# Kernel tuning notes

Measured on AMD Instinct MI355X. Metric: run time of the kernel, lower is better.

The kernel has to match this reference:

```python
import jax, jax.numpy as jnp
import numpy as np
from jax import lax

N = 5000            # number of detections
FEAT = 1024         # last-layer feature dim; 1024 + 9 engineered feats = indim 1033
DIMS = [FEAT + 9, 1000, 600, 300, 150, 1]
IOU_THRESH = 0.5
EPS = 2.220446049250313e-16  # sys.float_info.epsilon


def setup_inputs() -> dict:
    key = jax.random.key(0)
    ks = jax.random.split(key, 8 + 3 * len(DIMS))
    H, W = 800.0, 1333.0
    cx = jax.random.uniform(ks[0], (N,), minval=0.0, maxval=W)
    cy = jax.random.uniform(ks[1], (N,), minval=0.0, maxval=H)
    bw = jax.random.uniform(ks[2], (N,), minval=20.0, maxval=250.0)
    bh = jax.random.uniform(ks[3], (N,), minval=20.0, maxval=250.0)
    x1 = jnp.clip(cx - bw / 2, 0.0, W - 2)
    y1 = jnp.clip(cy - bh / 2, 0.0, H - 2)
    x2 = jnp.clip(cx + bw / 2, x1 + 1, W)
    y2 = jnp.clip(cy + bh / 2, y1 + 1, H)
    inp = {
        'multi_bboxes': jnp.stack([x1, y1, x2, y2], axis=1),
        'cls_score': jax.random.uniform(ks[4], (N, 2)),
        'last_layer_feats': jax.random.normal(ks[5], (N, FEAT)),
        'img_shape': jnp.array([H, W], jnp.float32),
    }
    # PermEqui2_mean params: Gamma (weight+bias) and Lambda (weight only)
    ki = 6
    for i, (din, dout) in enumerate(zip(DIMS[:-1], DIMS[1:])):
        s = 1.0 / np.sqrt(din)
        inp[f'Wg{i+1}'] = jax.random.uniform(ks[ki], (dout, din), minval=-s, maxval=s); ki += 1
        inp[f'bg{i+1}'] = jax.random.uniform(ks[ki], (dout,), minval=-s, maxval=s); ki += 1
        inp[f'Wl{i+1}'] = jax.random.uniform(ks[ki], (dout, din), minval=-s, maxval=s); ki += 1
    return inp


def _greedy_cluster(ious, thresh):
    # Sequential greedy IoU clustering (NMS-like). assign[i] = index of cluster seed.
    n = ious.shape[0]

    def step(carry, inp):
        is_c, assign = carry
        j, row = inp
        seed = is_c[j]
        hit = row > thresh
        member = seed & hit & is_c
        assign = jnp.where(member, j, assign)
        is_c = is_c & ~(seed & hit)
        return (is_c, assign), None

    init = (jnp.ones(n, bool), jnp.zeros(n, jnp.int32))
    (_, assign), _ = lax.scan(step, init, (jnp.arange(n, dtype=jnp.int32), ious))
    return assign


def _forward(multi_bboxes, cls_score, last_layer_feats, img_shape, params):
    n = multi_bboxes.shape[0]
    scores = cls_score[:, 1]
    order = jnp.argsort(-scores)
    scores = scores[order]
    bboxes = multi_bboxes[order]
    feats = last_layer_feats[order]

    x1, y1, x2, y2 = bboxes[:, 0], bboxes[:, 1], bboxes[:, 2], bboxes[:, 3]
    # pairwise IoU with the +1 pixel convention from bbox_overlaps
    iw = jnp.clip(jnp.minimum(x2[:, None], x2[None, :]) - jnp.maximum(x1[:, None], x1[None, :]) + 1, 0)
    ih = jnp.clip(jnp.minimum(y2[:, None], y2[None, :]) - jnp.maximum(y1[:, None], y1[None, :]) + 1, 0)
    area = (x2 - x1 + 1) * (y2 - y1 + 1)
    overlap = iw * ih
    ious = overlap / (area[:, None] + area[None, :] - overlap)

    assign = _greedy_cluster(lax.stop_gradient(ious), IOU_THRESH)
    counts = jax.ops.segment_sum(jnp.ones(n, jnp.float32), assign, num_segments=n)
    cden = jnp.maximum(counts, 1.0)

    Himg, Wimg = img_shape[0], img_shape[1]
    # source double-normalizes: width = (x2/W - x1/W)/W, height = (y2/H - y1/H)/H
    width = (x2 / Wimg - x1 / Wimg) / Wimg
    height = (y2 / Himg - y1 / Himg) / Himg
    areaf = width * height
    ar = width / (height + EPS)
    x = jnp.concatenate([
        bboxes, feats,
        width[:, None], height[:, None], ar[:, None], areaf[:, None], scores[:, None],
    ], axis=1)  # [n, 1033]

    def perm_equi(x, Wg, bg, Wl):
        # xm = per-set mean; x*Gamma^T + b - (xm*Lambda^T), gathered back per box
        xm = jax.ops.segment_sum(x, assign, num_segments=n) / cden[:, None]
        return x @ Wg.T + bg - (xm @ Wl.T)[assign]

    for i in range(5):
        x = jax.nn.elu(perm_equi(x, params[f'Wg{i+1}'], params[f'bg{i+1}'], params[f'Wl{i+1}']))

    # source skips singleton sets (nonzero().squeeze() -> 0-dim): mask them out
    valid = counts[assign] >= 2.0
    return jnp.where(valid[:, None], x, 0.0)  # [n, 1] per-box set logits


def reference(multi_bboxes, cls_score, last_layer_feats, img_shape,
              Wg1, bg1, Wl1, Wg2, bg2, Wl2, Wg3, bg3, Wl3,
              Wg4, bg4, Wl4, Wg5, bg5, Wl5):
    params = {'Wg1': Wg1, 'bg1': bg1, 'Wl1': Wl1, 'Wg2': Wg2, 'bg2': bg2, 'Wl2': Wl2,
              'Wg3': Wg3, 'bg3': bg3, 'Wl3': Wl3, 'Wg4': Wg4, 'bg4': bg4, 'Wl4': Wl4,
              'Wg5': Wg5, 'bg5': bg5, 'Wl5': Wl5}
    return _forward(multi_bboxes, cls_score, last_layer_feats, img_shape, params)
```

## Files before the change

kernel.cpp:

```cpp
#include <hip/hip_runtime.h>
#include <cstdint>
#include <cstddef>

#define N_BOX 5000
#define NW    80
#define LDX   1040
#define LDZ   2048
#define LDYM  1000
#define LDW   1040
#define LDAB  2080
#define NCHUNK ((N_BOX + 63) / 64)
#define RT    ((N_BOX + 255) / 256)

typedef short bf16x8 __attribute__((ext_vector_type(8)));
typedef float f32x4v __attribute__((ext_vector_type(4)));
typedef unsigned short u16x8 __attribute__((ext_vector_type(8)));

__device__ __forceinline__ float fence_f(float x) { asm volatile("" : "+v"(x)); return x; }

__device__ __forceinline__ unsigned short f2bf(float x) {
    unsigned u = __builtin_bit_cast(unsigned, x);
    unsigned r = (u + 0x7FFFu + ((u >> 16) & 1u)) >> 16;
    return (unsigned short)r;
}
__device__ __forceinline__ float bf2f(unsigned short h) {
    unsigned u = ((unsigned)h) << 16;
    return __builtin_bit_cast(float, u);
}

__global__ void rank_partial_kernel(const float* __restrict__ cls, int* __restrict__ rank) {
    __shared__ float sj[256];
    int t = threadIdx.x;
    int jbase = blockIdx.y * 256;
    int jg = jbase + t;
    sj[t] = (jg < N_BOX) ? cls[2 * jg + 1] : 0.0f;
    __syncthreads();
    int i = blockIdx.x * 256 + t;
    if (i >= N_BOX) return;
    float si = cls[2 * i + 1];
    int jmax = (N_BOX - jbase < 256) ? (N_BOX - jbase) : 256;
    int r = 0;
    for (int k = 0; k < jmax; ++k) {
        float sjv = sj[k];
        int j = jbase + k;
        r += (sjv > si) || (sjv == si && j < i);
    }
    atomicAdd(&rank[i], r);
}

__global__ void rank_scatter_kernel(const int* __restrict__ rank, int* __restrict__ ord) {
    int i = blockIdx.x * blockDim.x + threadIdx.x;
    if (i < N_BOX) ord[rank[i]] = i;
}

__global__ void gather_kernel(const float* __restrict__ bb, const float* __restrict__ cls,
                              const float* __restrict__ feats, const float* __restrict__ img,
                              const int* __restrict__ ord,
                              float* __restrict__ X0, float* __restrict__ sb,
                              unsigned short* __restrict__ A2) {
    int r = blockIdx.x;
    if (r >= N_BOX) {
        unsigned short* dst = A2 + (size_t)r * LDAB;
        for (int k = threadIdx.x; k < 2048; k += blockDim.x) dst[k] = 0;
        return;
    }
    int i = ord[r];
    float x1 = bb[4 * i + 0], y1 = bb[4 * i + 1], x2 = bb[4 * i + 2], y2 = bb[4 * i + 3];
    float H = img[0], W = img[1];
    float sc = cls[2 * i + 1];
    if (threadIdx.x == 0) {
        sb[0 * N_BOX + r] = x1;
        sb[1 * N_BOX + r] = y1;
        sb[2 * N_BOX + r] = x2;
        sb[3 * N_BOX + r] = y2;
        sb[4 * N_BOX + r] = (x2 - x1 + 1.0f) * (y2 - y1 + 1.0f);
        sb[5 * N_BOX + r] = sc;
    }
    float width  = (x2 / W - x1 / W) / W;
    float height = (y2 / H - y1 / H) / H;
    float ar     = width / (height + 2.220446049250313e-16f);
    float areaf  = width * height;
    float* row = X0 + (size_t)r * LDX;
    unsigned short* a2row = A2 + (size_t)r * LDAB;
    for (int o = threadIdx.x; o < LDX; o += blockDim.x) {
        float v;
        if (o < 4)          v = (o == 0) ? x1 : (o == 1) ? y1 : (o == 2) ? x2 : y2;
        else if (o < 1028)  v = feats[(size_t)i * 1024 + (o - 4)];
        else if (o == 1028) v = width;
        else if (o == 1029) v = height;
        else if (o == 1030) v = ar;
        else if (o == 1031) v = areaf;
        else if (o == 1032) v = sc;
        else                v = 0.0f;
        row[o] = v;
        if (o >= 4 && o < 1028) {
            int k = o - 4;
            unsigned short hi = f2bf(v);
            a2row[k] = hi;
            a2row[1024 + k] = f2bf(v - bf2f(hi));
        }
    }
}

__global__ void mask_kernel(const float* __restrict__ sb, unsigned long long* __restrict__ mask,
                            unsigned long long* __restrict__ diag, int* __restrict__ counts) {
    int j = blockIdx.x;
    if (threadIdx.x == 0) counts[j] = 0;
    const float* X1 = sb;
    const float* Y1 = sb + N_BOX;
    const float* X2 = sb + 2 * N_BOX;
    const float* Y2 = sb + 3 * N_BOX;
    const float* AR = sb + 4 * N_BOX;
    float xj1 = X1[j], yj1 = Y1[j], xj2 = X2[j], yj2 = Y2[j], aj = AR[j];
    int lane = threadIdx.x & 63;
    int wave = threadIdx.x >> 6;
    int nwav = blockDim.x >> 6;
    int dw = j >> 6;
    for (int w = wave; w < NW; w += nwav) {
        int i = w * 64 + lane;
        bool pred = false;
        if (i < N_BOX) {
            float iw = fmaxf(fminf(xj2, X2[i]) - fmaxf(xj1, X1[i]) + 1.0f, 0.0f);
            float ih = fmaxf(fminf(yj2, Y2[i]) - fmaxf(yj1, Y1[i]) + 1.0f, 0.0f);
            float ov = fence_f(iw * ih);
            float denom = fence_f((aj + AR[i]) - ov);
            pred = (ov / denom) > 0.5f;
        }
        unsigned long long b = __ballot(pred);
        if (lane == 0) {
            mask[(size_t)j * NW + w] = b;
            if (w == dw) diag[j] = b;
        }
    }
}

__device__ __forceinline__ void nms_body(const unsigned long long* __restrict__ mask,
                                         const unsigned long long* __restrict__ diag,
                                         unsigned long long* __restrict__ keep,
                                         unsigned long long* supp,
                                         unsigned long long* keep_sh,
                                         unsigned long long* rem_sh,
                                         unsigned long long* kb_sh) {
    int tid = threadIdx.x;
    int l = tid & 63;
    int w = tid >> 6;
    if (tid < 80) supp[tid] = 0ULL;
    unsigned long long dg = 0ULL, dg_next = 0ULL;
    if (w == 0) dg = diag[l];
    __syncthreads();
    for (int c = 0; c < NCHUNK; ++c) {
        if (w == 0) {
            unsigned long long curv = supp[c];
            unsigned clo = __builtin_amdgcn_readfirstlane((unsigned)curv);
            unsigned chi = __builtin_amdgcn_readfirstlane((unsigned)(curv >> 32));
            unsigned long long cur = ((unsigned long long)chi << 32) | clo;
            int jmax = (N_BOX - c * 64 < 64) ? (N_BOX - c * 64) : 64;
            unsigned long long valid = (jmax >= 64) ? ~0ULL : ((1ULL << jmax) - 1ULL);
            unsigned long long rem = ~cur & valid;
            if (l == 0) *rem_sh = rem;
        }
        __syncthreads();
        unsigned long long rem0 = *rem_sh;
        unsigned long long a0 = 0, a1 = 0, a2 = 0, a3 = 0, a4 = 0;
        unsigned long long b0 = 0, b1 = 0, b2 = 0, b3 = 0, b4 = 0;
        unsigned mym = 0;
        int base = (w - 1) * 5;
        if (w > 0) {
            mym = (base < 64) ? (unsigned)((rem0 >> base) & 31ULL) : 0u;
            const unsigned long long* rowp = mask + (size_t)(c * 64 + base) * NW;
            if (mym & 1u)  { a0 = rowp[0 * NW + l]; b0 = (l < 16) ? rowp[0 * NW + 64 + l] : 0ULL; }
            if (mym & 2u)  { a1 = rowp[1 * NW + l]; b1 = (l < 16) ? rowp[1 * NW + 64 + l] : 0ULL; }
            if (mym & 4u)  { a2 = rowp[2 * NW + l]; b2 = (l < 16) ? rowp[2 * NW + 64 + l] : 0ULL; }
            if (mym & 8u)  { a3 = rowp[3 * NW + l]; b3 = (l < 16) ? rowp[3 * NW + 64 + l] : 0ULL; }
            if (mym & 16u) { a4 = rowp[4 * NW + l]; b4 = (l < 16) ? rowp[4 * NW + 64 + l] : 0ULL; }
            asm volatile("" : "+v"(a0), "+v"(a1), "+v"(a2), "+v"(a3), "+v"(a4),
                             "+v"(b0), "+v"(b1), "+v"(b2), "+v"(b3), "+v"(b4));
        } else {
            if (c + 1 < NCHUNK) dg_next = diag[(size_t)(c + 1) * 64 + l];
            unsigned rlo = __builtin_amdgcn_readfirstlane((unsigned)rem0);
            unsigned rhi = __builtin_amdgcn_readfirstlane((unsigned)(rem0 >> 32));
            unsigned long long remS = ((unsigned long long)rhi << 32) | rlo;
            unsigned long long kb = 0ULL;
            while (remS) {
                int jj = __builtin_ctzll(remS);
                kb |= 1ULL << jj;
                unsigned dlo = __builtin_amdgcn_readlane((unsigned)dg, jj);
                unsigned dhi = __builtin_amdgcn_readlane((unsigned)(dg >> 32), jj);
                unsigned long long dj = ((unsigned long long)dhi << 32) | dlo;
                remS &= ~dj;
                remS &= ~(1ULL << jj);
            }
            if (l == 0) { *kb_sh = kb; keep_sh[c] = kb; }
        }
        __syncthreads();
        if (w > 0 && mym) {
            unsigned long long kb = *kb_sh;
            unsigned kw = ((unsigned)((kb >> base) & 31ULL)) & mym;
            if (kw & 1u)  { atomicOr(&supp[l], a0); if (l < 16) atomicOr(&supp[64 + l], b0); }
            if (kw & 2u)  { atomicOr(&supp[l], a1); if (l < 16) atomicOr(&supp[64 + l], b1); }
            if (kw & 4u)  { atomicOr(&supp[l], a2); if (l < 16) atomicOr(&supp[64 + l], b2); }
            if (kw & 8u)  { atomicOr(&supp[l], a3); if (l < 16) atomicOr(&supp[64 + l], b3); }
            if (kw & 16u) { atomicOr(&supp[l], a4); if (l < 16) atomicOr(&supp[64 + l], b4); }
        }
        if (w == 0) dg = dg_next;
        __syncthreads();
    }
    if (tid < NCHUNK) keep[tid] = keep_sh[tid];
}

__global__ __launch_bounds__(1024) void nms_scan_kernel(const unsigned long long* __restrict__ mask,
                                                        const unsigned long long* __restrict__ diag,
                                                        unsigned long long* __restrict__ keep) {
    __shared__ unsigned long long supp[80];
    __shared__ unsigned long long keep_sh[NCHUNK];
    __shared__ unsigned long long rem_sh;
    __shared__ unsigned long long kb_sh;
    nms_body(mask, diag, keep, supp, keep_sh, &rem_sh, &kb_sh);
}

__device__ __forceinline__ void wconv_row(const float* __restrict__ Wg, const float* __restrict__ Wl,
                                          unsigned short* __restrict__ B2, int n, int tid2,
                                          int dout, int din, int K16) {
    unsigned short* dst = B2 + (size_t)n * LDAB;
    if (n >= 2 * dout) {
        for (int k = tid2; k < K16; k += 256) dst[k] = 0;
        return;
    }
    const float* src = (n < dout) ? (Wg + (size_t)n * din) : (Wl + (size_t)(n - dout) * din);
    for (int k = tid2; k < K16; k += 256) {
        float x = (k < din) ? src[k] : 0.0f;
        dst[k] = f2bf(x);
    }
}

__global__ __launch_bounds__(1024) void nms_gemm_fused(const unsigned long long* __restrict__ mask,
                                                       const unsigned long long* __restrict__ diag,
                                                       unsigned long long* __restrict__ keep,
                                                       const unsigned short* __restrict__ A2,
                                                       const unsigned short* __restrict__ B2,
                                                       float* __restrict__ C, int KT, int Nn,
                                                       int MTiles,
                                                       const float* __restrict__ X0,
                                                       float* __restrict__ E9, float* __restrict__ W9,
                                                       const float* __restrict__ Wg1, const float* __restrict__ Wl1,
                                                       const float* __restrict__ Wg0full, const float* __restrict__ Wl0full,
                                                       unsigned short* __restrict__ B2_1,
                                                       const float* __restrict__ Wg2, const float* __restrict__ Wl2,
                                                       unsigned short* __restrict__ B2_2,
                                                       const float* __restrict__ Wg3, const float* __restrict__ Wl3,
                                                       unsigned short* __restrict__ B2_3) {
    __shared__ __align__(16) unsigned short AsBuf[2 * 8192];
    __shared__ __align__(16) unsigned short BsBuf[2 * 8192];
    int tid = threadIdx.x;
    int b = blockIdx.x;
    if (b == 0) {
        unsigned long long* supp    = (unsigned long long*)AsBuf;
        unsigned long long* keep_sh = supp + 80;
        unsigned long long* rem_sh  = keep_sh + NCHUNK;
        unsigned long long* kb_sh   = rem_sh + 1;
        nms_body(mask, diag, keep, supp, keep_sh, rem_sh, kb_sh);
        return;
    }
    int NG = MTiles * 8;
    if (b <= NG) {
        int t = b - 1;
        size_t bm = (size_t)(t % MTiles) * 256;
        size_t bn = (size_t)(t / MTiles) * 256;
        int lane = tid & 63;
        int wavef = tid >> 6;
        int wr = wavef >> 2, wc = wavef & 3;

        f32x4v acc[4][4];
#pragma unroll
        for (int i = 0; i < 4; ++i)
#pragma unroll
            for (int j = 0; j < 4; ++j) acc[i][j] = (f32x4v){0.f, 0.f, 0.f, 0.f};

        const unsigned short* gA = A2 + (bm + wavef * 16 + (lane & 15)) * (size_t)LDAB + (lane >> 4) * 8;
        const unsigned short* gB = B2 + (bn + wavef * 16 + (lane & 15)) * (size_t)LDAB + (lane >> 4) * 8;
        unsigned ldsoff = (unsigned)((wavef * 64 + lane) * 16);

#define FSTAGE(T, BUF)                                                                             \
        {                                                                                          \
            size_t ko = (size_t)(T) * 32;                                                          \
            __builtin_amdgcn_global_load_lds(                                                      \
                (const __attribute__((address_space(1))) void*)(gA + ko),                          \
                (__attribute__((address_space(3))) void*)((char*)AsBuf + (BUF) * 16384 + ldsoff),  \
                16, 0, 0);                                                                         \
            __builtin_amdgcn_global_load_lds(                                                      \
                (const __attribute__((address_space(1))) void*)(gB + ko),                          \
                (__attribute__((address_space(3))) void*)((char*)BsBuf + (BUF) * 16384 + ldsoff),  \
                16, 0, 0);                                                                         \
        }

        FSTAGE(0, 0);
        for (int kt = 0; kt < KT; ++kt) {
            int cur = kt & 1;
            if (kt + 1 < KT) {
                FSTAGE(kt + 1, cur ^ 1);
                asm volatile("s_waitcnt vmcnt(2)" ::: "memory");
            } else {
                asm volatile("s_waitcnt vmcnt(0)" ::: "memory");
            }
            asm volatile("s_barrier" ::: "memory");
            bf16x8 af[4], bf[4];
#pragma unroll
            for (int f4 = 0; f4 < 4; ++f4) {
                af[f4] = *(const bf16x8*)((const char*)AsBuf + cur * 16384 + ((wr * 4 + f4) * 64 + lane) * 16);
                bf[f4] = *(const bf16x8*)((const char*)BsBuf + cur * 16384 + ((wc * 4 + f4) * 64 + lane) * 16);
            }
#pragma unroll
            for (int i = 0; i < 4; ++i)
#pragma unroll
                for (int j = 0; j < 4; ++j)
                    acc[i][j] = __builtin_amdgcn_mfma_f32_16x16x32_bf16(af[i], bf[j], acc[i][j], 0, 0, 0);
            asm volatile("s_barrier" ::: "memory");
        }
#undef FSTAGE

#pragma unroll
        for (int i = 0; i < 4; ++i) {
            int r0 = (int)bm + wr * 64 + i * 16 + (lane >> 4) * 4;
#pragma unroll
            for (int j = 0; j < 4; ++j) {
                int col = (int)bn + wc * 64 + j * 16 + (lane & 15);
                if (col < Nn) {
#pragma unroll
                    for (int e = 0; e < 4; ++e) {
                        int r = r0 + e;
                        if (r < N_BOX) C[(size_t)r * LDZ + col] = acc[i][j][e];
                    }
                }
            }
        }
        return;
    }
    int rb = b - 1 - NG;
    const int cq[9] = {0, 1, 2, 3, 1028, 1029, 1030, 1031, 1032};
    if (rb < 5) {
        int r = rb * 1024 + tid;
        if (r < 5120) {
            float* dst = E9 + (size_t)r * 12;
#pragma unroll
            for (int q = 0; q < 9; ++q) dst[q] = (r < N_BOX) ? X0[(size_t)r * LDX + cq[q]] : 0.0f;
            dst[9] = dst[10] = dst[11] = 0.0f;
        }
        return;
    }
    rb -= 5;
    if (rb < 2) {
        int n = rb * 1024 + tid;
        if (n < 2048) {
            float* dst = W9 + (size_t)n * 12;
            const float* src = (n < 1000) ? (Wg0full + (size_t)n * 1033)
                             : (n < 2000) ? (Wl0full + (size_t)(n - 1000) * 1033) : nullptr;
#pragma unroll
            for (int q = 0; q < 9; ++q) dst[q] = src ? src[cq[q]] : 0.0f;
            dst[9] = dst[10] = dst[11] = 0.0f;
        }
        return;
    }
    rb -= 2;
    int rowl = tid >> 8;
    int tid2 = tid & 255;
    if (rb < 320) {
        int n = rb * 4 + rowl;
        if (n < 1280) wconv_row(Wg1, Wl1, B2_1, n, tid2, 600, 1000, 1024);
        return;
    }
    rb -= 320;
    if (rb < 160) {
        int n = rb * 4 + rowl;
        if (n < 640) wconv_row(Wg2, Wl2, B2_2, n, tid2, 300, 600, 608);
        return;
    }
    rb -= 160;
    {
        int n = rb * 4 + rowl;
        if (n < 384) wconv_row(Wg3, Wl3, B2_3, n, tid2, 150, 300, 320);
        return;
    }
}

__global__ void z9_assign_kernel(float* __restrict__ Z, const float* __restrict__ E9,
                                 const float* __restrict__ W9, int Nn,
                                 const unsigned long long* __restrict__ mask,
                                 const unsigned long long* __restrict__ keep,
                                 int* __restrict__ assign, int* __restrict__ counts) {
    int b = blockIdx.x;
    if (b < N_BOX) {
        int r = b;
        float e[9];
#pragma unroll
        for (int q = 0; q < 9; ++q) e[q] = E9[(size_t)r * 12 + q];
        for (int o = threadIdx.x; o < Nn; o += blockDim.x) {
            const float* w = W9 + (size_t)o * 12;
            float s = 0.0f;
#pragma unroll
            for (int q = 0; q < 9; ++q) s += e[q] * w[q];
            Z[(size_t)r * LDZ + o] += s;
        }
        return;
    }
    int i = (b - N_BOX) * 256 + threadIdx.x;
    if (i >= N_BOX) return;
    for (int w = 0; w < NCHUNK; ++w) {
        unsigned long long m = mask[(size_t)i * NW + w] & keep[w];
        if (m) {
            int j = w * 64 + __builtin_ctzll(m);
            assign[i] = j;
            atomicAdd(&counts[j], 1);
            return;
        }
    }
}

__global__ void assign_kernel(const unsigned long long* __restrict__ mask,
                              const unsigned long long* __restrict__ keep,
                              int* __restrict__ assign, int* __restrict__ counts) {
    int i = blockIdx.x * blockDim.x + threadIdx.x;
    if (i >= N_BOX) return;
    for (int w = 0; w < NCHUNK; ++w) {
        unsigned long long m = mask[(size_t)i * NW + w] & keep[w];
        if (m) {
            int j = w * 64 + __builtin_ctzll(m);
            assign[i] = j;
            atomicAdd(&counts[j], 1);
            return;
        }
    }
}

__global__ __launch_bounds__(1024) void scan_kernel(const int* __restrict__ counts, int* __restrict__ offs) {
    __shared__ int part[1024];
    int t = threadIdx.x;
    int base = t * 5;
    int c[5];
    int s = 0;
#pragma unroll
    for (int k = 0; k < 5; ++k) {
        int idx = base + k;
        c[k] = (idx < N_BOX) ? counts[idx] : 0;
        s += c[k];
    }
    part[t] = s;
    __syncthreads();
    for (int d = 1; d < 1024; d <<= 1) {
        int v = part[t];
        int u = (t >= d) ? part[t - d] : 0;
        __syncthreads();
        part[t] = v + u;
        __syncthreads();
    }
    int run = (t > 0) ? part[t - 1] : 0;
#pragma unroll
    for (int k = 0; k < 5; ++k) {
        int idx = base + k;
        if (idx < N_BOX) offs[idx] = run;
        run += c[k];
    }
}

__global__ void rankscatter_kernel(const int* __restrict__ assign, const int* __restrict__ offs,
                                   int* __restrict__ members) {
    __shared__ int a[N_BOX];
    int tid = threadIdx.x;
    for (int t = tid; t < N_BOX; t += blockDim.x) a[t] = assign[t];
    __syncthreads();
    int i = blockIdx.x * blockDim.x + tid;
    if (i >= N_BOX) return;
    int ai = a[i];
    int r = 0;
    for (int k = 0; k < i; ++k) r += (a[k] == ai);
    members[offs[ai] + r] = i;
}

__global__ void wconv_kernel(const float* __restrict__ Wg, const float* __restrict__ Wl,
                             unsigned short* __restrict__ B2, int dout, int din_src,
                             int din_eff, int colOff, int K16eff) {
    int n = blockIdx.x;
    unsigned short* dst = B2 + (size_t)n * LDAB;
    int K2 = 2 * K16eff;
    if (n >= 2 * dout) {
        for (int k = threadIdx.x; k < K2; k += blockDim.x) dst[k] = 0;
        return;
    }
    const float* src = (n < dout) ? (Wg + (size_t)n * din_src) : (Wl + (size_t)(n - dout) * din_src);
    for (int k = threadIdx.x; k < K2; k += blockDim.x) {
        int ks = (k >= K16eff) ? (k - K16eff) : k;
        float x = (ks < din_eff) ? src[colOff + ks] : 0.0f;
        dst[k] = f2bf(x);
    }
}

__global__ __launch_bounds__(256, 4) void gemm_mfma(const unsigned short* __restrict__ A2,
                                                    const unsigned short* __restrict__ B2,
                                                    float* __restrict__ C, int KT, int Nn) {
    __shared__ unsigned short AsBuf[2 * 4096];
    __shared__ unsigned short BsBuf[2 * 4096];
    int tid = threadIdx.x;
    int lane = tid & 63;
    int wave = tid >> 6;
    int wr = wave >> 1, wc = wave & 1;
    size_t bm = (size_t)blockIdx.x * 128;
    size_t bn = (size_t)blockIdx.y * 128;

    f32x4v acc[4][4];
#pragma unroll
    for (int i = 0; i < 4; ++i)
#pragma unroll
        for (int j = 0; j < 4; ++j) acc[i][j] = (f32x4v){0.f, 0.f, 0.f, 0.f};

    const unsigned short* gA[2];
    const unsigned short* gB[2];
    unsigned ldsoff[2];
#pragma unroll
    for (int q = 0; q < 2; ++q) {
        int f = q * 4 + wave;
        int grow = f * 16 + (lane & 15);
        int gcol = (lane >> 4) * 8;
        gA[q] = A2 + (bm + grow) * (size_t)LDAB + gcol;
        gB[q] = B2 + (bn + grow) * (size_t)LDAB + gcol;
        ldsoff[q] = (unsigned)((f * 64 + lane) * 16);
    }

#define STAGE(T, BUF)                                                                              \
    {                                                                                              \
        size_t ko = (size_t)(T) * 32;                                                              \
        _Pragma("unroll") for (int q = 0; q < 2; ++q) {                                            \
            __builtin_amdgcn_global_load_lds(                                                      \
                (const __attribute__((address_space(1))) void*)(gA[q] + ko),                       \
                (__attribute__((address_space(3))) void*)((char*)AsBuf + (BUF) * 8192 + ldsoff[q]),\
                16, 0, 0);                                                                         \
            __builtin_amdgcn_global_load_lds(                                                      \
                (const __attribute__((address_space(1))) void*)(gB[q] + ko),                       \
                (__attribute__((address_space(3))) void*)((char*)BsBuf + (BUF) * 8192 + ldsoff[q]),\
                16, 0, 0);                                                                         \
        }                                                                                          \
    }

    STAGE(0, 0);
    for (int kt = 0; kt < KT; ++kt) {
        int cur = kt & 1;
        if (kt + 1 < KT) {
            STAGE(kt + 1, cur ^ 1);
            asm volatile("s_waitcnt vmcnt(4)" ::: "memory");
        } else {
            asm volatile("s_waitcnt vmcnt(0)" ::: "memory");
        }
        asm volatile("s_barrier" ::: "memory");
        bf16x8 af[4], bf[4];
#pragma unroll
        for (int f4 = 0; f4 < 4; ++f4) {
            af[f4] = *(const bf16x8*)((const char*)AsBuf + cur * 8192 + ((wr * 4 + f4) * 64 + lane) * 16);
            bf[f4] = *(const bf16x8*)((const char*)BsBuf + cur * 8192 + ((wc * 4 + f4) * 64 + lane) * 16);
        }
#pragma unroll
        for (int i = 0; i < 4; ++i)
#pragma unroll
            for (int j = 0; j < 4; ++j)
                acc[i][j] = __builtin_amdgcn_mfma_f32_16x16x32_bf16(af[i], bf[j], acc[i][j], 0, 0, 0);
        asm volatile("s_barrier" ::: "memory");
    }
#undef STAGE

#pragma unroll
    for (int i = 0; i < 4; ++i) {
        int r0 = (int)bm + wr * 64 + i * 16 + (lane >> 4) * 4;
#pragma unroll
        for (int j = 0; j < 4; ++j) {
            int col = (int)bn + wc * 64 + j * 16 + (lane & 15);
            if (col < Nn) {
#pragma unroll
                for (int e = 0; e < 4; ++e) {
                    int r = r0 + e;
                    if (r < N_BOX) C[(size_t)r * LDZ + col] = acc[i][j][e];
                }
            }
        }
    }
}

__global__ void wcat_kernel(const float* __restrict__ Wg, const float* __restrict__ Wl,
                            float* __restrict__ Wc, int dout, int din, int K16) {
    int row = blockIdx.x;
    const float* src = (row < dout) ? (Wg + (size_t)row * din) : (Wl + (size_t)(row - dout) * din);
    float* dst = Wc + (size_t)row * LDW;
    for (int k = threadIdx.x; k < K16; k += blockDim.x)
        dst[k] = (k < din) ? src[k] : 0.0f;
}

__global__ __launch_bounds__(256) void gemm_nt(const float* __restrict__ A, const float* __restrict__ B,
                                               float* __restrict__ C, int M, int Nn, int K16) {
    __shared__ float As[16][64];
    __shared__ float Bs[16][64];
    int bm = blockIdx.x * 64;
    int bn = blockIdx.y * 64;
    int tid = threadIdx.x;
    int row = tid & 63;
    int kq  = tid >> 6;
    int tx  = tid & 15;
    int ty  = tid >> 4;
    float acc[4][4] = {};
    for (int k0 = 0; k0 < K16; k0 += 16) {
        float4 av = make_float4(0.f, 0.f, 0.f, 0.f);
        float4 bv = make_float4(0.f, 0.f, 0.f, 0.f);
        if (bm + row < M)  av = *(const float4*)&A[(size_t)(bm + row) * LDX + k0 + kq * 4];
        if (bn + row < Nn) bv = *(const float4*)&B[(size_t)(bn + row) * LDW + k0 + kq * 4];
        __syncthreads();
        As[kq * 4 + 0][row] = av.x; As[kq * 4 + 1][row] = av.y;
        As[kq * 4 + 2][row] = av.z; As[kq * 4 + 3][row] = av.w;
        Bs[kq * 4 + 0][row] = bv.x; Bs[kq * 4 + 1][row] = bv.y;
        Bs[kq * 4 + 2][row] = bv.z; Bs[kq * 4 + 3][row] = bv.w;
        __syncthreads();
#pragma unroll
        for (int kk = 0; kk < 16; ++kk) {
            float4 a = *(const float4*)&As[kk][ty * 4];
            float4 b = *(const float4*)&Bs[kk][tx * 4];
            float aa[4] = {a.x, a.y, a.z, a.w};
            float bb[4] = {b.x, b.y, b.z, b.w};
#pragma unroll
            for (int i = 0; i < 4; ++i)
#pragma unroll
                for (int jx = 0; jx < 4; ++jx) acc[i][jx] += aa[i] * bb[jx];
        }
    }
#pragma unroll
    for (int i = 0; i < 4; ++i) {
        int r = bm + ty * 4 + i;
        if (r >= M) break;
#pragma unroll
        for (int jx = 0; jx < 4; ++jx) {
            int ccol = bn + tx * 4 + jx;
            if (ccol < Nn) C[(size_t)r * LDZ + ccol] = acc[i][jx];
        }
    }
}

__global__ void segmean_kernel(const float* __restrict__ Z, int dout,
                               const int* __restrict__ counts, const int* __restrict__ offs,
                               const int* __restrict__ members, float* __restrict__ ym) {
    int j = blockIdx.x;
    int cnt = counts[j];
    if (cnt == 0) return;
    int off = offs[j];
    float fc = (float)cnt;
    for (int o = threadIdx.x; o < dout; o += blockDim.x) {
        float s = 0.0f;
        for (int m = 0; m < cnt; ++m) {
            int i = members[off + m];
            s += Z[(size_t)i * LDZ + dout + o];
        }
        ym[(size_t)j * LDYM + o] = s / fc;
    }
}

__global__ void combine_kernel(const float* __restrict__ Z, const float* __restrict__ bg,
                               const float* __restrict__ ym, const int* __restrict__ assign,
                               float* __restrict__ Xout, int dout, int doutPad) {
    int r = blockIdx.x;
    int a = assign[r];
    float* dst = Xout + (size_t)r * LDX;
    for (int o = threadIdx.x; o < doutPad; o += blockDim.x) {
        float v = 0.0f;
        if (o < dout) {
            float z = Z[(size_t)r * LDZ + o] + bg[o] - ym[(size_t)a * LDYM + o];
            v = (z > 0.0f) ? z : expm1f(z);
        }
        dst[o] = v;
    }
}

__global__ void combine_fused_kernel(const float* __restrict__ Z, const float* __restrict__ bg,
                                     const float* __restrict__ ym, const int* __restrict__ assign,
                                     unsigned short* __restrict__ A2, int dout, int K16next) {
    int r = blockIdx.x;
    int a = assign[r];
    unsigned short* dst = A2 + (size_t)r * LDAB;
    for (int o = threadIdx.x; o < K16next; o += blockDim.x) {
        float v = 0.0f;
        if (o < dout) {
            float z = Z[(size_t)r * LDZ + o] + bg[o] - ym[(size_t)a * LDYM + o];
            v = (z > 0.0f) ? z : expm1f(z);
        }
        dst[o] = f2bf(v);
    }
}

__global__ void l4a_kernel(const float* __restrict__ X, const float* __restrict__ Wg,
                           const float* __restrict__ Wl, float* __restrict__ zg,
                           float* __restrict__ zl) {
    int r = blockIdx.x * blockDim.x + threadIdx.x;
    if (r >= N_BOX) return;
    const float* row = X + (size_t)r * LDX;
    float sg = 0.0f, sl = 0.0f;
    for (int k = 0; k < 150; ++k) {
        float x = row[k];
        sg += x * Wg[k];
        sl += x * Wl[k];
    }
    zg[r] = sg;
    zl[r] = sl;
}

__global__ __launch_bounds__(64) void l4b_kernel(const float* __restrict__ zl,
                                                 const int* __restrict__ counts,
                                                 const int* __restrict__ offs,
                                                 const int* __restrict__ members,
                                                 float* __restrict__ ym4) {
    int j = blockIdx.x;
    int cnt = counts[j];
    if (cnt == 0) return;
    int off = offs[j];
    int l = threadIdx.x;
    float s = 0.0f;
    for (int m = l; m < cnt; m += 64) s += zl[members[off + m]];
#pragma unroll
    for (int d = 1; d < 64; d <<= 1) s += __shfl_xor(s, d);
    if (l == 0) ym4[j] = s / (float)cnt;
}

__global__ void l4c_kernel(const float* __restrict__ zg, const float* __restrict__ ym4,
                           const float* __restrict__ bg, const int* __restrict__ assign,
                           const int* __restrict__ counts, float* __restrict__ out) {
    int r = blockIdx.x * blockDim.x + threadIdx.x;
    if (r >= N_BOX) return;
    int a = assign[r];
    float z = zg[r] + bg[0] - ym4[a];
    float v = (z > 0.0f) ? z : expm1f(z);
    out[r] = (counts[a] >= 2) ? v : 0.0f;
}

__global__ void final_kernel(const float* __restrict__ X, const int* __restrict__ assign,
                             const int* __restrict__ counts, float* __restrict__ out) {
    int r = blockIdx.x * blockDim.x + threadIdx.x;
    if (r >= N_BOX) return;
    out[r] = (counts[assign[r]] >= 2) ? X[(size_t)r * LDX] : 0.0f;
}

extern "C" void kernel_launch(void* const* d_in, const int* in_sizes, int n_in,
                              void* d_out, int out_size, void* d_ws, size_t ws_size,
                              hipStream_t stream) {
    const float* bb    = (const float*)d_in[0];
    const float* cls   = (const float*)d_in[1];
    const float* feats = (const float*)d_in[2];
    const float* img   = (const float*)d_in[3];

    char* ws = (char*)d_ws;
    size_t off = 0;
    auto alloc = [&](size_t bytes) -> void* {
        void* p = ws + off;
        off += (bytes + 255) & ~(size_t)255;
        return p;
    };
    int*   ord     = (int*)alloc((size_t)N_BOX * 4);
    int*   rankb   = (int*)alloc((size_t)N_BOX * 4);
    float* sb      = (float*)alloc((size_t)6 * N_BOX * 4);
    int*   assign  = (int*)alloc((size_t)N_BOX * 4);
    int*   counts  = (int*)alloc((size_t)N_BOX * 4);
    int*   offsb   = (int*)alloc((size_t)N_BOX * 4);
    int*   members = (int*)alloc((size_t)N_BOX * 4);
    unsigned long long* mask = (unsigned long long*)alloc((size_t)(NCHUNK * 64) * NW * 8);
    unsigned long long* diag = (unsigned long long*)alloc((size_t)NCHUNK * 64 * 8);
    unsigned long long* keep = (unsigned long long*)alloc((size_t)NCHUNK * 8 + 1024);
    float* Xa = (float*)alloc((size_t)N_BOX * LDX * 4);
    float* Xb = (float*)alloc((size_t)N_BOX * LDX * 4);
    float* Z  = (float*)alloc((size_t)N_BOX * LDZ * 4);
    float* ym = (float*)alloc((size_t)N_BOX * LDYM * 4);
    float* Wc = (float*)alloc((size_t)2000 * LDW * 4);
    unsigned short* A2   = (unsigned short*)alloc((size_t)5120 * LDAB * 2);
    unsigned short* B2_0 = (unsigned short*)alloc((size_t)2048 * LDAB * 2);
    unsigned short* B2_1 = (unsigned short*)alloc((size_t)1280 * LDAB * 2);
    unsigned short* B2_2 = (unsigned short*)alloc((size_t)640 * LDAB * 2);
    unsigned short* B2_3 = (unsigned short*)alloc((size_t)384 * LDAB * 2);
    float* E9 = (float*)alloc((size_t)5120 * 12 * 4);
    float* W9 = (float*)alloc((size_t)2048 * 12 * 4);
    float* zg  = (float*)alloc((size_t)N_BOX * 4);
    float* zl  = (float*)alloc((size_t)N_BOX * 4);
    float* ym4 = (float*)alloc((size_t)N_BOX * 4);
    bool use_mfma = (off <= ws_size);

    hipMemsetAsync(rankb, 0, (size_t)N_BOX * 4, stream);
    rank_partial_kernel<<<dim3(RT, RT), dim3(256), 0, stream>>>(cls, rankb);
    rank_scatter_kernel<<<dim3(RT), dim3(256), 0, stream>>>(rankb, ord);
    gather_kernel<<<dim3(5120), dim3(256), 0, stream>>>(bb, cls, feats, img, ord, Xa, sb, A2);
    mask_kernel<<<dim3(N_BOX), dim3(256), 0, stream>>>(sb, mask, diag, counts);

    const int dins[5]  = {1033, 1000, 600, 300, 150};
    const int douts[5] = {1000, 600, 300, 150, 1};
    const int K16s[4]  = {1024, 1024, 608, 320};
    const int KTs[4]   = {64, 32, 19, 10};
    unsigned short* B2L[4] = {B2_0, B2_1, B2_2, B2_3};

    if (use_mfma) {
        wconv_kernel<<<dim3(2048), dim3(256), 0, stream>>>((const float*)d_in[4], (const float*)d_in[6],
                                                           B2_0, 1000, 1033, 1024, 4, 1024);
        nms_gemm_fused<<<dim3(744), dim3(1024), 0, stream>>>(
            mask, diag, keep, A2, B2_0, Z, KTs[0], 2000, 20,
            Xa, E9, W9,
            (const float*)d_in[7], (const float*)d_in[9],
            (const float*)d_in[4], (const float*)d_in[6],
            B2_1,
            (const float*)d_in[10], (const float*)d_in[12], B2_2,
            (const float*)d_in[13], (const float*)d_in[15], B2_3);
        z9_assign_kernel<<<dim3(N_BOX + RT), dim3(256), 0, stream>>>(Z, E9, W9, 2000,
                                                                     mask, keep, assign, counts);
        scan_kernel<<<dim3(1), dim3(1024), 0, stream>>>(counts, offsb);
        rankscatter_kernel<<<dim3(RT), dim3(256), 0, stream>>>(assign, offsb, members);

        for (int L = 0; L < 4; ++L) {
            const float* bg = (const float*)d_in[5 + 3 * L];
            int dout = douts[L];
            int N2 = 2 * dout;
            if (L > 0) {
                int Ntiles = (N2 + 127) >> 7;
                gemm_mfma<<<dim3(40, Ntiles), dim3(256), 0, stream>>>(A2, B2L[L], Z, KTs[L], N2);
            }
            segmean_kernel<<<dim3(N_BOX), dim3(256), 0, stream>>>(Z, dout, counts, offsb, members, ym);
            if (L < 3) {
                combine_fused_kernel<<<dim3(N_BOX), dim3(256), 0, stream>>>(Z, bg, ym, assign, A2,
                                                                            dout, K16s[L + 1]);
            } else {
                combine_kernel<<<dim3(N_BOX), dim3(256), 0, stream>>>(Z, bg, ym, assign, Xa, dout, 160);
            }
        }
        l4a_kernel<<<dim3(RT), dim3(256), 0, stream>>>(Xa, (const float*)d_in[16],
                                                       (const float*)d_in[18], zg, zl);
        l4b_kernel<<<dim3(N_BOX), dim3(64), 0, stream>>>(zl, counts, offsb, members, ym4);
        l4c_kernel<<<dim3(RT), dim3(256), 0, stream>>>(zg, ym4, (const float*)d_in[17],
                                                       assign, counts, (float*)d_out);
    } else {
        nms_scan_kernel<<<dim3(1), dim3(1024), 0, stream>>>(mask, diag, keep);
        assign_kernel<<<dim3(RT), dim3(256), 0, stream>>>(mask, keep, assign, counts);
        scan_kernel<<<dim3(1), dim3(1024), 0, stream>>>(counts, offsb);
        rankscatter_kernel<<<dim3(RT), dim3(256), 0, stream>>>(assign, offsb, members);
        for (int L = 0; L < 5; ++L) {
            const float* Wg = (const float*)d_in[4 + 3 * L];
            const float* bg = (const float*)d_in[5 + 3 * L];
            const float* Wl = (const float*)d_in[6 + 3 * L];
            int din = dins[L], dout = douts[L];
            int K16 = (din + 15) & ~15;
            int N2 = 2 * dout;
            int doutPad = (dout + 15) & ~15;
            float* Xin  = (L % 2 == 0) ? Xa : Xb;
            float* Xout = (L % 2 == 0) ? Xb : Xa;
            wcat_kernel<<<dim3(N2), dim3(256), 0, stream>>>(Wg, Wl, Wc, dout, din, K16);
            gemm_nt<<<dim3((N_BOX + 63) / 64, (N2 + 63) / 64), dim3(256), 0, stream>>>(Xin, Wc, Z, N_BOX, N2, K16);
            segmean_kernel<<<dim3(N_BOX), dim3(256), 0, stream>>>(Z, dout, counts, offsb, members, ym);
            combine_kernel<<<dim3(N_BOX), dim3(256), 0, stream>>>(Z, bg, ym, assign, Xout, dout, doutPad);
        }
        final_kernel<<<dim3(RT), dim3(256), 0, stream>>>(Xb, assign, counts, (float*)d_out);
    }
}
```

Measured before the change: 467.4 us.

## Pipeline greedy NMS scan with lagged suppression and next-chunk diagonal patch

Restructures the sequential NMS clustering loop so that the worker waves apply the suppression rows of chunk c-1 while wave 0 resolves chunk c. This cuts the per-chunk barriers from three to one and removes the shared rem/kb handoff. Correctness is kept by having mask_kernel also store the next-chunk (super-diagonal) mask block. Wave 0 ORs the rows of its kept boxes via shuffle reduction into a patch for the next chunk. This adds a memset and a shuffle reduction per chunk and makes the mask loads conditional on the keep bits only.

```diff
diff --git a/kernel.cpp b/kernel.cpp
--- a/kernel.cpp
+++ b/kernel.cpp
@@ -103,7 +103,7 @@
 }
 
 __global__ void mask_kernel(const float* __restrict__ sb, unsigned long long* __restrict__ mask,
-                            unsigned long long* __restrict__ diag, int* __restrict__ counts) {
+                            unsigned long long* __restrict__ diag2, int* __restrict__ counts) {
     int j = blockIdx.x;
     if (threadIdx.x == 0) counts[j] = 0;
     const float* X1 = sb;
@@ -115,7 +115,8 @@
     int lane = threadIdx.x & 63;
     int wave = threadIdx.x >> 6;
     int nwav = blockDim.x >> 6;
-    int dw = j >> 6;
+    int c = j >> 6;
+    int lj = j & 63;
     for (int w = wave; w < NW; w += nwav) {
         int i = w * 64 + lane;
         bool pred = false;
@@ -129,93 +130,89 @@
         unsigned long long b = __ballot(pred);
         if (lane == 0) {
             mask[(size_t)j * NW + w] = b;
-            if (w == dw) diag[j] = b;
+            if (w == c)     diag2[(size_t)c * 128 + lj] = b;
+            if (w == c + 1) diag2[(size_t)c * 128 + 64 + lj] = b;
         }
     }
 }
 
 __device__ __forceinline__ void nms_body(const unsigned long long* __restrict__ mask,
-                                         const unsigned long long* __restrict__ diag,
+                                         const unsigned long long* __restrict__ diag2,
                                          unsigned long long* __restrict__ keep,
                                          unsigned long long* supp,
-                                         unsigned long long* keep_sh,
-                                         unsigned long long* rem_sh,
-                                         unsigned long long* kb_sh) {
+                                         unsigned long long* keep_sh) {
     int tid = threadIdx.x;
     int l = tid & 63;
     int w = tid >> 6;
+    int base = (w - 1) * 5;
     if (tid < 80) supp[tid] = 0ULL;
-    unsigned long long dg = 0ULL, dg_next = 0ULL;
-    if (w == 0) dg = diag[l];
+    unsigned long long dg = 0, sd = 0, dgn = 0, sdn = 0, patch = 0;
+    if (w == 0) { dg = diag2[l]; sd = diag2[64 + l]; }
     __syncthreads();
     for (int c = 0; c < NCHUNK; ++c) {
         if (w == 0) {
             unsigned long long curv = supp[c];
             unsigned clo = __builtin_amdgcn_readfirstlane((unsigned)curv);
             unsigned chi = __builtin_amdgcn_readfirstlane((unsigned)(curv >> 32));
-            unsigned long long cur = ((unsigned long long)chi << 32) | clo;
+            unsigned long long cur = (((unsigned long long)chi << 32) | clo) | patch;
             int jmax = (N_BOX - c * 64 < 64) ? (N_BOX - c * 64) : 64;
             unsigned long long valid = (jmax >= 64) ? ~0ULL : ((1ULL << jmax) - 1ULL);
-            unsigned long long rem = ~cur & valid;
-            if (l == 0) *rem_sh = rem;
-        }
-        __syncthreads();
-        unsigned long long rem0 = *rem_sh;
-        unsigned long long a0 = 0, a1 = 0, a2 = 0, a3 = 0, a4 = 0;
-        unsigned long long b0 = 0, b1 = 0, b2 = 0, b3 = 0, b4 = 0;
-        unsigned mym = 0;
-        int base = (w - 1) * 5;
-        if (w > 0) {
-            mym = (base < 64) ? (unsigned)((rem0 >> base) & 31ULL) : 0u;
-            const unsigned long long* rowp = mask + (size_t)(c * 64 + base) * NW;
-            if (mym & 1u)  { a0 = rowp[0 * NW + l]; b0 = (l < 16) ? rowp[0 * NW + 64 + l] : 0ULL; }
-            if (mym & 2u)  { a1 = rowp[1 * NW + l]; b1 = (l < 16) ? rowp[1 * NW + 64 + l] : 0ULL; }
-            if (mym & 4u)  { a2 = rowp[2 * NW + l]; b2 = (l < 16) ? rowp[2 * NW + 64 + l] : 0ULL; }
-            if (mym & 8u)  { a3 = rowp[3 * NW + l]; b3 = (l < 16) ? rowp[3 * NW + 64 + l] : 0ULL; }
-            if (mym & 16u) { a4 = rowp[4 * NW + l]; b4 = (l < 16) ? rowp[4 * NW + 64 + l] : 0ULL; }
-            asm volatile("" : "+v"(a0), "+v"(a1), "+v"(a2), "+v"(a3), "+v"(a4),
-                             "+v"(b0), "+v"(b1), "+v"(b2), "+v"(b3), "+v"(b4));
-        } else {
-            if (c + 1 < NCHUNK) dg_next = diag[(size_t)(c + 1) * 64 + l];
-            unsigned rlo = __builtin_amdgcn_readfirstlane((unsigned)rem0);
-            unsigned rhi = __builtin_amdgcn_readfirstlane((unsigned)(rem0 >> 32));
+            unsigned rlo = __builtin_amdgcn_readfirstlane((unsigned)(~cur & valid));
+            unsigned rhi = __builtin_amdgcn_readfirstlane((unsigned)((~cur & valid) >> 32));
             unsigned long long remS = ((unsigned long long)rhi << 32) | rlo;
-            unsigned long long kb = 0ULL;
+            unsigned long long kbv = 0ULL;
             while (remS) {
                 int jj = __builtin_ctzll(remS);
-                kb |= 1ULL << jj;
+                kbv |= 1ULL << jj;
                 unsigned dlo = __builtin_amdgcn_readlane((unsigned)dg, jj);
                 unsigned dhi = __builtin_amdgcn_readlane((unsigned)(dg >> 32), jj);
-                unsigned long long dj = ((unsigned long long)dhi << 32) | dlo;
-                remS &= ~dj;
+                remS &= ~(((unsigned long long)dhi << 32) | dlo);
                 remS &= ~(1ULL << jj);
             }
-            if (l == 0) { *kb_sh = kb; keep_sh[c] = kb; }
+            if (l == 0) keep_sh[c] = kbv;
+            unsigned long long contrib = ((kbv >> l) & 1ULL) ? sd : 0ULL;
+            unsigned pl = (unsigned)contrib, ph = (unsigned)(contrib >> 32);
+#pragma unroll
+            for (int d = 1; d < 64; d <<= 1) {
+                pl |= __shfl_xor(pl, d);
+                ph |= __shfl_xor(ph, d);
+            }
+            patch = ((unsigned long long)ph << 32) | pl;
+            if (c + 1 < NCHUNK) {
+                dgn = diag2[(size_t)(c + 1) * 128 + l];
+                sdn = diag2[(size_t)(c + 1) * 128 + 64 + l];
+            }
+        } else if (c >= 1) {
+            unsigned long long kbw = keep_sh[c - 1];
+            unsigned kw = (base < 64) ? (unsigned)((kbw >> base) & 31ULL) : 0u;
+            if (kw) {
+                const unsigned long long* rowp = mask + (size_t)((c - 1) * 64 + base) * NW;
+                unsigned long long a0 = 0, a1 = 0, a2 = 0, a3 = 0, a4 = 0;
+                unsigned long long b0 = 0, b1 = 0, b2 = 0, b3 = 0, b4 = 0;
+                if (kw & 1u)  { a0 = rowp[0 * NW + l]; b0 = (l < 16) ? rowp[0 * NW + 64 + l] : 0ULL; }
+                if (kw & 2u)  { a1 = rowp[1 * NW + l]; b1 = (l < 16) ? rowp[1 * NW + 64 + l] : 0ULL; }
+                if (kw & 4u)  { a2 = rowp[2 * NW + l]; b2 = (l < 16) ? rowp[2 * NW + 64 + l] : 0ULL; }
+                if (kw & 8u)  { a3 = rowp[3 * NW + l]; b3 = (l < 16) ? rowp[3 * NW + 64 + l] : 0ULL; }
+                if (kw & 16u) { a4 = rowp[4 * NW + l]; b4 = (l < 16) ? rowp[4 * NW + 64 + l] : 0ULL; }
+                if (kw & 1u)  { atomicOr(&supp[l], a0); if (l < 16) atomicOr(&supp[64 + l], b0); }
+                if (kw & 2u)  { atomicOr(&supp[l], a1); if (l < 16) atomicOr(&supp[64 + l], b1); }
+                if (kw & 4u)  { atomicOr(&supp[l], a2); if (l < 16) atomicOr(&supp[64 + l], b2); }
+                if (kw & 8u)  { atomicOr(&supp[l], a3); if (l < 16) atomicOr(&supp[64 + l], b3); }
+                if (kw & 16u) { atomicOr(&supp[l], a4); if (l < 16) atomicOr(&supp[64 + l], b4); }
+            }
         }
         __syncthreads();
-        if (w > 0 && mym) {
-            unsigned long long kb = *kb_sh;
-            unsigned kw = ((unsigned)((kb >> base) & 31ULL)) & mym;
-            if (kw & 1u)  { atomicOr(&supp[l], a0); if (l < 16) atomicOr(&supp[64 + l], b0); }
-            if (kw & 2u)  { atomicOr(&supp[l], a1); if (l < 16) atomicOr(&supp[64 + l], b1); }
-            if (kw & 4u)  { atomicOr(&supp[l], a2); if (l < 16) atomicOr(&supp[64 + l], b2); }
-            if (kw & 8u)  { atomicOr(&supp[l], a3); if (l < 16) atomicOr(&supp[64 + l], b3); }
-            if (kw & 16u) { atomicOr(&supp[l], a4); if (l < 16) atomicOr(&supp[64 + l], b4); }
-        }
-        if (w == 0) dg = dg_next;
-        __syncthreads();
+        if (w == 0) { dg = dgn; sd = sdn; }
     }
     if (tid < NCHUNK) keep[tid] = keep_sh[tid];
 }
 
 __global__ __launch_bounds__(1024) void nms_scan_kernel(const unsigned long long* __restrict__ mask,
-                                                        const unsigned long long* __restrict__ diag,
+                                                        const unsigned long long* __restrict__ diag2,
                                                         unsigned long long* __restrict__ keep) {
     __shared__ unsigned long long supp[80];
     __shared__ unsigned long long keep_sh[NCHUNK];
-    __shared__ unsigned long long rem_sh;
-    __shared__ unsigned long long kb_sh;
-    nms_body(mask, diag, keep, supp, keep_sh, &rem_sh, &kb_sh);
+    nms_body(mask, diag2, keep, supp, keep_sh);
 }
 
 __device__ __forceinline__ void wconv_row(const float* __restrict__ Wg, const float* __restrict__ Wl,
@@ -234,7 +231,7 @@
 }
 
 __global__ __launch_bounds__(1024) void nms_gemm_fused(const unsigned long long* __restrict__ mask,
-                                                       const unsigned long long* __restrict__ diag,
+                                                       const unsigned long long* __restrict__ diag2,
                                                        unsigned long long* __restrict__ keep,
                                                        const unsigned short* __restrict__ A2,
                                                        const unsigned short* __restrict__ B2,
@@ -256,9 +253,7 @@
     if (b == 0) {
         unsigned long long* supp    = (unsigned long long*)AsBuf;
         unsigned long long* keep_sh = supp + 80;
-        unsigned long long* rem_sh  = keep_sh + NCHUNK;
-        unsigned long long* kb_sh   = rem_sh + 1;
-        nms_body(mask, diag, keep, supp, keep_sh, rem_sh, kb_sh);
+        nms_body(mask, diag2, keep, supp, keep_sh);
         return;
     }
     int NG = MTiles * 8;
@@ -760,9 +755,9 @@
     int*   counts  = (int*)alloc((size_t)N_BOX * 4);
     int*   offsb   = (int*)alloc((size_t)N_BOX * 4);
     int*   members = (int*)alloc((size_t)N_BOX * 4);
-    unsigned long long* mask = (unsigned long long*)alloc((size_t)(NCHUNK * 64) * NW * 8);
-    unsigned long long* diag = (unsigned long long*)alloc((size_t)NCHUNK * 64 * 8);
-    unsigned long long* keep = (unsigned long long*)alloc((size_t)NCHUNK * 8 + 1024);
+    unsigned long long* mask  = (unsigned long long*)alloc((size_t)(NCHUNK * 64) * NW * 8);
+    unsigned long long* diag2 = (unsigned long long*)alloc((size_t)NCHUNK * 128 * 8);
+    unsigned long long* keep  = (unsigned long long*)alloc((size_t)NCHUNK * 8 + 1024);
     float* Xa = (float*)alloc((size_t)N_BOX * LDX * 4);
     float* Xb = (float*)alloc((size_t)N_BOX * LDX * 4);
     float* Z  = (float*)alloc((size_t)N_BOX * LDZ * 4);
@@ -781,10 +776,11 @@
     bool use_mfma = (off <= ws_size);
 
     hipMemsetAsync(rankb, 0, (size_t)N_BOX * 4, stream);
+    hipMemsetAsync(diag2, 0, (size_t)NCHUNK * 128 * 8, stream);
     rank_partial_kernel<<<dim3(RT, RT), dim3(256), 0, stream>>>(cls, rankb);
     rank_scatter_kernel<<<dim3(RT), dim3(256), 0, stream>>>(rankb, ord);
     gather_kernel<<<dim3(5120), dim3(256), 0, stream>>>(bb, cls, feats, img, ord, Xa, sb, A2);
-    mask_kernel<<<dim3(N_BOX), dim3(256), 0, stream>>>(sb, mask, diag, counts);
+    mask_kernel<<<dim3(N_BOX), dim3(256), 0, stream>>>(sb, mask, diag2, counts);
 
     const int dins[5]  = {1033, 1000, 600, 300, 150};
     const int douts[5] = {1000, 600, 300, 150, 1};
@@ -796,7 +792,7 @@
         wconv_kernel<<<dim3(2048), dim3(256), 0, stream>>>((const float*)d_in[4], (const float*)d_in[6],
                                                            B2_0, 1000, 1033, 1024, 4, 1024);
         nms_gemm_fused<<<dim3(744), dim3(1024), 0, stream>>>(
-            mask, diag, keep, A2, B2_0, Z, KTs[0], 2000, 20,
+            mask, diag2, keep, A2, B2_0, Z, KTs[0], 2000, 20,
             Xa, E9, W9,
             (const float*)d_in[7], (const float*)d_in[9],
             (const float*)d_in[4], (const float*)d_in[6],
@@ -830,7 +826,7 @@
         l4c_kernel<<<dim3(RT), dim3(256), 0, stream>>>(zg, ym4, (const float*)d_in[17],
                                                        assign, counts, (float*)d_out);
     } else {
-        nms_scan_kernel<<<dim3(1), dim3(1024), 0, stream>>>(mask, diag, keep);
+        nms_scan_kernel<<<dim3(1), dim3(1024), 0, stream>>>(mask, diag2, keep);
         assign_kernel<<<dim3(RT), dim3(256), 0, stream>>>(mask, keep, assign, counts);
         scan_kernel<<<dim3(1), dim3(1024), 0, stream>>>(counts, offsb);
         rankscatter_kernel<<<dim3(RT), dim3(256), 0, stream>>>(assign, offsb, members);
```

Result: no change. 470.8 us (+0.7%).
